# Optimization experiments

Hardware: AMD Instinct MI355X
Metric: run time of the kernel (lower is better)

Reference implementation:

```python
import jax, jax.numpy as jnp
import numpy as np

B, S, D, H, FF = 2, 2048, 1024, 16, 4096
DH = D // H
EPS = 1e-5


def rmsnorm(x, g):
    rms = jnp.sqrt(jnp.mean(x * x, axis=-1, keepdims=True) + EPS)
    return x / rms * g


def gelu(x):
    return x * 0.5 * (1.0 + jax.lax.erf(x / np.float32(np.sqrt(2.0))))


def setup_inputs() -> dict:
    key = jax.random.key(0)
    ks = jax.random.split(key, 9)
    sd = np.float32(1.0 / np.sqrt(D))
    sf = np.float32(1.0 / np.sqrt(FF))
    return {
        'x': jax.random.normal(ks[0], (B, S, D), jnp.float32),
        'wq': jax.random.normal(ks[1], (D, D), jnp.float32) * sd,
        'wk': jax.random.normal(ks[2], (D, D), jnp.float32) * sd,
        'wv': jax.random.normal(ks[3], (D, D), jnp.float32) * sd,
        'wo': jax.random.normal(ks[4], (D, D), jnp.float32) * sd,
        'w1': jax.random.normal(ks[5], (FF, D), jnp.float32) * sd,
        'w2': jax.random.normal(ks[6], (D, FF), jnp.float32) * sf,
        'g1': jax.random.uniform(ks[7], (D,), jnp.float32),
        'g2': jax.random.uniform(ks[8], (D,), jnp.float32),
    }


def reference(x, wq, wk, wv, wo, w1, w2, g1, g2):
    b, s, d = x.shape
    h = rmsnorm(x, g1)
    # torch Linear: y = x @ W.T ; split heads -> [b, s, H, DH]
    q = jnp.einsum('bsd,ed->bse', h, wq).reshape(b, s, H, DH)
    k = jnp.einsum('bsd,ed->bse', h, wk).reshape(b, s, H, DH)
    v = jnp.einsum('bsd,ed->bse', h, wv).reshape(b, s, H, DH)
    score = jnp.einsum('bqhd,bkhd->bhqk', q, k) / np.float32(np.sqrt(DH))
    causal = jnp.triu(jnp.ones((s, s), bool), 1)  # strictly upper = masked
    score = score + jnp.where(causal, jnp.float32(-1e9), jnp.float32(0.0))
    attn_w = jax.nn.softmax(score, axis=-1)
    o = jnp.einsum('bhqk,bkhd->bqhd', attn_w, v).reshape(b, s, d)
    attn_out = jnp.einsum('bsd,ed->bse', o, wo)
    x2 = attn_out + x
    h2 = rmsnorm(x2, g2)
    ffn = jnp.einsum('bsf,df->bsd', gelu(jnp.einsum('bsd,fd->bsf', h2, w1)), w2)
    return ffn + x2
```

## Files before the change

kernel.cpp:

```cpp
#include <hip/hip_runtime.h>
#include <cstdint>

#define B_ 2
#define S_ 2048
#define D_ 1024
#define H_ 16
#define DH_ 64
#define FF_ 4096
#define M_TOK (B_ * S_)

typedef __attribute__((ext_vector_type(8))) short short8;
typedef __attribute__((ext_vector_type(4))) float f32x4;
typedef __attribute__((ext_vector_type(4))) unsigned short us4;

typedef unsigned short u16;

#define SCL 0.18033688011112042f

__device__ __forceinline__ float bf2f(u16 u) {
  union { uint32_t u; float f; } x;
  x.u = ((uint32_t)u) << 16;
  return x.f;
}
__device__ __forceinline__ u16 f2bf(float f) {
  union { float f; uint32_t u; } x;
  x.f = f;
  uint32_t r = x.u + 0x7FFFu + ((x.u >> 16) & 1u);
  return (u16)(r >> 16);
}

__device__ __forceinline__ uint32_t pack2bf(float a, float b) {
  union { float f; uint32_t u; } x, y;
  x.f = a; y.f = b;
#if __has_builtin(__builtin_amdgcn_perm)
  return __builtin_amdgcn_perm(y.u + 0x8000u, x.u + 0x8000u, 0x07060302u);
#else
  return ((x.u + 0x8000u) >> 16) | ((y.u + 0x8000u) & 0xFFFF0000u);
#endif
}

__device__ __forceinline__ void gl_lds16(const void* g, void* l) {
  __builtin_amdgcn_global_load_lds(
      (const __attribute__((address_space(1))) uint32_t*)(uintptr_t)g,
      (__attribute__((address_space(3))) uint32_t*)(uintptr_t)l, 16, 0, 0);
}

__device__ __forceinline__ float gelu_f(float v) {
  const float y = 0.7978845608f * (v + 0.044715f * v * v * v);
  const float t = exp2f(y * 2.885390082f);
  const float th = 1.0f - 2.0f * __builtin_amdgcn_rcpf(t + 1.0f);
  return 0.5f * v * (1.0f + th);
}

#define MEG 1048576
#define PREP_CVT 12288

__global__ __launch_bounds__(256) void prep_k(const float* __restrict__ wq, const float* __restrict__ wk,
                                              const float* __restrict__ wv, const float* __restrict__ wo,
                                              const float* __restrict__ w1, const float* __restrict__ w2,
                                              u16* __restrict__ wqkv, u16* __restrict__ wob,
                                              u16* __restrict__ w1b, u16* __restrict__ w2b,
                                              const float* __restrict__ X, const float* __restrict__ G,
                                              u16* __restrict__ Hout) {
  __shared__ float red[4];
  const int bid = blockIdx.x;
  const int tid = threadIdx.x;
  if (bid < PREP_CVT) {
    const int n = (bid * 256 + tid) * 4;
    const float* src;
    u16* dst;
    int off;
    if (n < 3 * MEG) {
      dst = wqkv; off = n;
      src = (n < MEG) ? wq + n : (n < 2 * MEG ? wk + (n - MEG) : wv + (n - 2 * MEG));
    } else if (n < 4 * MEG) {
      dst = wob; off = n - 3 * MEG; src = wo + off;
    } else if (n < 8 * MEG) {
      dst = w1b; off = n - 4 * MEG; src = w1 + off;
    } else {
      dst = w2b; off = n - 8 * MEG; src = w2 + off;
    }
    const float4 v = *(const float4*)src;
    us4 o;
    o[0] = f2bf(v.x); o[1] = f2bf(v.y); o[2] = f2bf(v.z); o[3] = f2bf(v.w);
    *(us4*)&dst[off] = o;
  } else {
    const int row = bid - PREP_CVT;
    const float4 xx = *(const float4*)&X[(size_t)row * D_ + tid * 4];
    float v[4] = {xx.x, xx.y, xx.z, xx.w};
    float s = 0.f;
#pragma unroll
    for (int i = 0; i < 4; ++i) s += v[i] * v[i];
#pragma unroll
    for (int d = 1; d < 64; d <<= 1) s += __shfl_xor(s, d);
    if ((tid & 63) == 0) red[tid >> 6] = s;
    __syncthreads();
    s = red[0] + red[1] + red[2] + red[3];
    const float scale = rsqrtf(s * (1.0f / (float)D_) + 1e-5f);
    const float4 gg = *(const float4*)&G[tid * 4];
    us4 o;
    o[0] = f2bf(v[0] * scale * gg.x);
    o[1] = f2bf(v[1] * scale * gg.y);
    o[2] = f2bf(v[2] * scale * gg.z);
    o[3] = f2bf(v[3] * scale * gg.w);
    *(us4*)&Hout[(size_t)row * D_ + tid * 4] = o;
  }
}

__global__ __launch_bounds__(256) void rmsnorm_wo_k(const u16* __restrict__ P0, const u16* __restrict__ P1,
                                                    const float* __restrict__ X, const float* __restrict__ G,
                                                    float* __restrict__ X2, u16* __restrict__ Hout) {
  const int row = blockIdx.x;
  const int tid = threadIdx.x;
  const size_t off = (size_t)row * D_ + tid * 4;
  const us4 p0 = *(const us4*)&P0[off];
  const us4 p1 = *(const us4*)&P1[off];
  const float4 xx = *(const float4*)&X[off];
  float v[4];
  v[0] = bf2f(p0[0]) + bf2f(p1[0]) + xx.x;
  v[1] = bf2f(p0[1]) + bf2f(p1[1]) + xx.y;
  v[2] = bf2f(p0[2]) + bf2f(p1[2]) + xx.z;
  v[3] = bf2f(p0[3]) + bf2f(p1[3]) + xx.w;
  *(float4*)&X2[off] = float4{v[0], v[1], v[2], v[3]};
  float s = 0.f;
#pragma unroll
  for (int i = 0; i < 4; ++i) s += v[i] * v[i];
#pragma unroll
  for (int d = 1; d < 64; d <<= 1) s += __shfl_xor(s, d);
  __shared__ float red[4];
  if ((tid & 63) == 0) red[tid >> 6] = s;
  __syncthreads();
  s = red[0] + red[1] + red[2] + red[3];
  const float scale = rsqrtf(s * (1.0f / (float)D_) + 1e-5f);
  const float4 gg = *(const float4*)&G[tid * 4];
  us4 o;
  o[0] = f2bf(v[0] * scale * gg.x);
  o[1] = f2bf(v[1] * scale * gg.y);
  o[2] = f2bf(v[2] * scale * gg.z);
  o[3] = f2bf(v[3] * scale * gg.w);
  *(us4*)&Hout[off] = o;
}

__global__ __launch_bounds__(256) void ffn2_red_k(const u16* __restrict__ Q0, const u16* __restrict__ Q1,
                                                  float* __restrict__ OUT) {
  const int i = (blockIdx.x * 256 + threadIdx.x) * 4;
  const us4 a = *(const us4*)&Q0[i];
  const us4 b = *(const us4*)&Q1[i];
  const float4 c = *(const float4*)&OUT[i];
  *(float4*)&OUT[i] = float4{bf2f(a[0]) + bf2f(b[0]) + c.x, bf2f(a[1]) + bf2f(b[1]) + c.y,
                             bf2f(a[2]) + bf2f(b[2]) + c.z, bf2f(a[3]) + bf2f(b[3]) + c.w};
}

template <int MODE>
__global__ __launch_bounds__(256) void gemm_bt_k(const u16* __restrict__ A,
                                                 const u16* __restrict__ W,
                                                 u16* __restrict__ C0, u16* __restrict__ C1,
                                                 u16* __restrict__ C2, int N, int K) {
  __shared__ alignas(16) u16 As[256 * 32];
  __shared__ alignas(16) u16 Bs[256 * 32];
  const int tid = threadIdx.x;
  const int wv = tid >> 6, lane = tid & 63;
  const int r = lane & 15, quad = lane >> 4;
  const int nx = gridDim.x;
  const int nwg = nx * gridDim.y;
  const int orig = blockIdx.x + nx * blockIdx.y;
  const int id = (orig & 7) * (nwg >> 3) + (orig >> 3);
  const int bn = (id % nx) * 128;
  const int bm = (id / nx) * 128;
  const int row0 = (wv >> 1) * 64, col0 = (wv & 1) * 64;

  f32x4 acc[4][4] = {};

  int sm[4], sh[4], sg[4];
#pragma unroll
  for (int jj = 0; jj < 4; ++jj) {
    const int c = wv * 256 + jj * 64 + lane;
    const int lr = c >> 2;
    sm[jj] = lr & 127;
    sh[jj] = lr >> 7;
    sg[jj] = (c & 3) ^ ((sm[jj] >> 1) & 3);
  }

  for (int k0 = 0; k0 < K; k0 += 64) {
#pragma unroll
    for (int jj = 0; jj < 4; ++jj) {
      const int l0 = (wv * 256 + jj * 64) * 8;
      gl_lds16(&A[(size_t)(bm + sm[jj]) * K + k0 + sh[jj] * 32 + sg[jj] * 8], &As[l0]);
      gl_lds16(&W[(size_t)(bn + sm[jj]) * K + k0 + sh[jj] * 32 + sg[jj] * 8], &Bs[l0]);
    }
    __syncthreads();
#pragma unroll
    for (int h = 0; h < 2; ++h) {
      short8 af[4], bf[4];
#pragma unroll
      for (int mt = 0; mt < 4; ++mt) {
        const int mr = row0 + mt * 16 + r;
        af[mt] = *(const short8*)&As[(mr + 128 * h) * 32 + (quad ^ ((mr >> 1) & 3)) * 8];
      }
#pragma unroll
      for (int nt = 0; nt < 4; ++nt) {
        const int nr = col0 + nt * 16 + r;
        bf[nt] = *(const short8*)&Bs[(nr + 128 * h) * 32 + (quad ^ ((nr >> 1) & 3)) * 8];
      }
#pragma unroll
      for (int mt = 0; mt < 4; ++mt)
#pragma unroll
        for (int nt = 0; nt < 4; ++nt)
          acc[mt][nt] = __builtin_amdgcn_mfma_f32_16x16x32_bf16(af[mt], bf[nt], acc[mt][nt], 0, 0, 0);
    }
    __syncthreads();
  }

  if constexpr (MODE == 2) {
#pragma unroll
    for (int mt = 0; mt < 4; ++mt)
#pragma unroll
      for (int nt = 0; nt < 4; ++nt)
#pragma unroll
        for (int i = 0; i < 4; ++i) {
          const int grow = bm + row0 + mt * 16 + quad * 4 + i;
          const int gcol = bn + col0 + nt * 16 + r;
          C0[(size_t)grow * N + gcol] = f2bf(gelu_f(acc[mt][nt][i]));
        }
  } else {
    if (bn < 2048) {
#pragma unroll
      for (int mt = 0; mt < 4; ++mt) {
        const int grow0 = bm + row0 + mt * 16 + quad * 4;
#pragma unroll
        for (int nt = 0; nt < 4; ++nt) {
          const int gcol = bn + col0 + nt * 16 + r;
          u16* dst = (gcol < 1024) ? C0 : C1;
          const float sc = (gcol < 1024) ? SCL : 1.0f;
          const int cc = gcol & 1023;
#pragma unroll
          for (int i = 0; i < 4; ++i)
            dst[(size_t)(grow0 + i) * 1024 + cc] = f2bf(acc[mt][nt][i] * sc);
        }
      }
    } else {
#pragma unroll
      for (int mtp = 0; mtp < 4; mtp += 2) {
        const int tok0 = bm + row0 + mtp * 16 + quad * 4;
#pragma unroll
        for (int nt = 0; nt < 4; ++nt) {
          const int vcol = bn + col0 + nt * 16 + r - 2048;
          const size_t vtrow = (size_t)((tok0 >> 11) * 16 + (vcol >> 6)) * 64 + (vcol & 63);
#pragma unroll
          for (int i = 0; i < 4; ++i) {
            const int s = (tok0 + i) & 2047;
            const uint32_t pk =
                (uint32_t)f2bf(acc[mtp][nt][i]) | ((uint32_t)f2bf(acc[mtp + 1][nt][i]) << 16);
            *(uint32_t*)&C2[vtrow * 2048 + s + (s & 15)] = pk;
          }
        }
      }
    }
  }
}

__global__ __launch_bounds__(256) void gemm_sk2_k(const u16* __restrict__ A,
                                                  const u16* __restrict__ W,
                                                  u16* __restrict__ P0, u16* __restrict__ P1,
                                                  int N, int K, int KS) {
  __shared__ alignas(16) u16 As[256 * 32];
  __shared__ alignas(16) u16 Bs[256 * 32];
  const int tid = threadIdx.x;
  const int wv = tid >> 6, lane = tid & 63;
  const int r = lane & 15, quad = lane >> 4;
  const int orig = blockIdx.x + 8 * (blockIdx.y + 32 * blockIdx.z);
  const int id = (orig & 7) * 64 + (orig >> 3);
  const int bn = (id & 7) * 128;
  const int bm = ((id >> 3) & 31) * 128;
  const int bz = id >> 8;
  const int row0 = (wv >> 1) * 64, col0 = (wv & 1) * 64;
  const int koff = bz * KS;
  u16* P = bz ? P1 : P0;

  f32x4 acc[4][4] = {};

  int sm[4], sh[4], sg[4];
#pragma unroll
  for (int jj = 0; jj < 4; ++jj) {
    const int c = wv * 256 + jj * 64 + lane;
    const int lr = c >> 2;
    sm[jj] = lr & 127;
    sh[jj] = lr >> 7;
    sg[jj] = (c & 3) ^ ((sm[jj] >> 1) & 3);
  }

  for (int k0 = koff; k0 < koff + KS; k0 += 64) {
#pragma unroll
    for (int jj = 0; jj < 4; ++jj) {
      const int l0 = (wv * 256 + jj * 64) * 8;
      gl_lds16(&A[(size_t)(bm + sm[jj]) * K + k0 + sh[jj] * 32 + sg[jj] * 8], &As[l0]);
      gl_lds16(&W[(size_t)(bn + sm[jj]) * K + k0 + sh[jj] * 32 + sg[jj] * 8], &Bs[l0]);
    }
    __syncthreads();
#pragma unroll
    for (int h = 0; h < 2; ++h) {
      short8 af[4], bf[4];
#pragma unroll
      for (int mt = 0; mt < 4; ++mt) {
        const int mr = row0 + mt * 16 + r;
        af[mt] = *(const short8*)&As[(mr + 128 * h) * 32 + (quad ^ ((mr >> 1) & 3)) * 8];
      }
#pragma unroll
      for (int nt = 0; nt < 4; ++nt) {
        const int nr = col0 + nt * 16 + r;
        bf[nt] = *(const short8*)&Bs[(nr + 128 * h) * 32 + (quad ^ ((nr >> 1) & 3)) * 8];
      }
#pragma unroll
      for (int mt = 0; mt < 4; ++mt)
#pragma unroll
        for (int nt = 0; nt < 4; ++nt)
          acc[mt][nt] = __builtin_amdgcn_mfma_f32_16x16x32_bf16(af[mt], bf[nt], acc[mt][nt], 0, 0, 0);
    }
    __syncthreads();
  }

#pragma unroll
  for (int mt = 0; mt < 4; ++mt)
#pragma unroll
    for (int nt = 0; nt < 4; ++nt)
#pragma unroll
      for (int i = 0; i < 4; ++i) {
        const int grow = bm + row0 + mt * 16 + quad * 4 + i;
        const int gcol = bn + col0 + nt * 16 + r;
        P[(size_t)grow * N + gcol] = f2bf(acc[mt][nt][i]);
      }
}

#define ATTN_BODY(BUF, J0, RINK, RINV, ROUTK, ROUTV, DO_PF, DO_WR)                                 \
  {                                                                                                \
    __syncthreads();                                                                               \
    if (DO_PF) {                                                                                   \
      ROUTK = *(const short8*)&Kb[(size_t)((J0) + 64 + krow) * D_ + kg * 8];                       \
      ROUTV = *(const short8*)&VTb[(size_t)vrow * 2048 + (J0) + 64 + vg * 8];                      \
    }                                                                                              \
    f32x4 z[2][2];                                                                                 \
    __builtin_amdgcn_s_setprio(1);                                                                 \
    _Pragma("unroll") for (int kt = 0; kt < 2; ++kt) {                                             \
      const short8 kf0 = *(const short8*)&Ks[BUF][(kt * 16 + r) * 72 + quad * 8];                  \
      const short8 kf1 = *(const short8*)&Ks[BUF][(kt * 16 + r) * 72 + 32 + quad * 8];             \
      _Pragma("unroll") for (int f = 0; f < 2; ++f) {                                              \
        f32x4 zz = {};                                                                             \
        zz = __builtin_amdgcn_mfma_f32_16x16x32_bf16(qf[f][0], kf0, zz, 0, 0, 0);                  \
        zz = __builtin_amdgcn_mfma_f32_16x16x32_bf16(qf[f][1], kf1, zz, 0, 0, 0);                  \
        z[f][kt] = zz;                                                                             \
      }                                                                                            \
    }                                                                                              \
    __builtin_amdgcn_s_setprio(0);                                                                 \
    const bool masked = ((J0) + 31 > m0);                                                          \
    _Pragma("unroll") for (int f = 0; f < 2; ++f) _Pragma("unroll") for (int i = 0; i < 4; ++i) {  \
      const int qrow = m0 + f * 16 + quad * 4 + i;                                                 \
      float v0 = z[f][0][i];                                                                       \
      float v1 = z[f][1][i];                                                                       \
      if (masked) {                                                                                \
        if ((J0) + r > qrow) v0 = -128.f;                                                          \
        if ((J0) + 16 + r > qrow) v1 = -128.f;                                                     \
      }                                                                                            \
      *(uint32_t*)&Psw[(f * 16 + quad * 4 + i) * 40 + r * 2] = pack2bf(exp2f(v0), exp2f(v1));      \
    }                                                                                              \
    asm volatile("s_waitcnt lgkmcnt(0)" ::: "memory");                                             \
    short8 vf[4];                                                                                  \
    _Pragma("unroll") for (int nt = 0; nt < 4; ++nt)                                               \
        vf[nt] = *(const short8*)&Vs[BUF][(nt * 16 + r) * 40 + quad * 8];                          \
    __builtin_amdgcn_s_setprio(1);                                                                 \
    _Pragma("unroll") for (int f = 0; f < 2; ++f) {                                                \
      const short8 pf = *(const short8*)&Psw[(f * 16 + r) * 40 + quad * 8];                        \
      _Pragma("unroll") for (int nt = 0; nt < 4; ++nt)                                             \
          oacc[f][nt] = __builtin_amdgcn_mfma_f32_16x16x32_bf16(pf, vf[nt], oacc[f][nt], 0, 0, 0); \
      lacc[f] = __builtin_amdgcn_mfma_f32_16x16x32_bf16(pf, onesv, lacc[f], 0, 0, 0);              \
    }                                                                                              \
    __builtin_amdgcn_s_setprio(0);                                                                 \
    if (DO_WR) {                                                                                   \
      *(short8*)&Ks[(BUF) ^ 1][krow * 72 + kg * 8] = RINK;                                         \
      *(short8*)&Vs[(BUF) ^ 1][vrow * 40 + vg * 8] = RINV;                                         \
    }                                                                                              \
  }

__global__ __launch_bounds__(256, 2) void attn_k(const u16* __restrict__ Q,
                                                 const u16* __restrict__ Kx,
                                                 const u16* __restrict__ VT,
                                                 u16* __restrict__ O) {
  __shared__ alignas(16) u16 Ks[2][32 * 72];
  __shared__ alignas(16) u16 Vs[2][64 * 40];
  __shared__ alignas(16) u16 Ps[4][32 * 40];

  const int tid = threadIdx.x;
  const int wv = tid >> 6, lane = tid & 63;
  const int r = lane & 15, quad = lane >> 4;

  const int i_ = blockIdx.x + 16 * blockIdx.y;
  const int w = i_ >> 8;
  const int j = i_ & 255;
  const int xcd = j & 7;
  const int u = j >> 3;
  const int bh = xcd * 4 + (u >> 3);
  const int s = u & 7;
  const int bx = w ? s : (15 - s);
  const int b = bh >> 4, hh = bh & 15;

  const int niter = (bx + 1) * 4;
  const int m0 = bx * 128 + wv * 32;
  const size_t base = (size_t)b * S_ * D_ + (size_t)hh * DH_;
  const u16* Qb = Q + base;
  const u16* Kb = Kx + base;
  const u16* VTb = VT + (size_t)bh * 64 * 2048;
  u16* Psw = &Ps[wv][0];

  short8 qf[2][2];
#pragma unroll
  for (int f = 0; f < 2; ++f) {
    qf[f][0] = *(const short8*)&Qb[(size_t)(m0 + f * 16 + r) * D_ + quad * 8];
    qf[f][1] = *(const short8*)&Qb[(size_t)(m0 + f * 16 + r) * D_ + 32 + quad * 8];
  }

  short8 onesv;
#pragma unroll
  for (int e = 0; e < 8; ++e) onesv[e] = (short)0x3F80;

  f32x4 oacc[2][4] = {};
  f32x4 lacc[2] = {};

  const int krow = tid >> 3, kg = tid & 7;
  const int vrow = tid >> 2, vg = tid & 3;

  *(short8*)&Ks[0][krow * 72 + kg * 8] = *(const short8*)&Kb[(size_t)krow * D_ + kg * 8];
  *(short8*)&Vs[0][vrow * 40 + vg * 8] = *(const short8*)&VTb[(size_t)vrow * 2048 + vg * 8];
  short8 kA, vA, kB, vB;
  kA = *(const short8*)&Kb[(size_t)(32 + krow) * D_ + kg * 8];
  vA = *(const short8*)&VTb[(size_t)vrow * 2048 + 32 + vg * 8];

  for (int it = 0; it < niter; it += 2) {
    const int j0 = it * 32;
    ATTN_BODY(0, j0, kA, vA, kB, vB, (it + 2 < niter), true);
    ATTN_BODY(1, j0 + 32, kB, vB, kA, vA, (it + 3 < niter), (it + 2 < niter));
  }

#pragma unroll
  for (int f = 0; f < 2; ++f) {
#pragma unroll
    for (int i = 0; i < 4; ++i) {
      const int qrow = m0 + f * 16 + quad * 4 + i;
      const float linv = 1.0f / lacc[f][i];
#pragma unroll
      for (int nt = 0; nt < 4; ++nt)
        O[base + (size_t)qrow * D_ + nt * 16 + r] = f2bf(oacc[f][nt][i] * linv);
    }
  }
}

extern "C" void kernel_launch(void* const* d_in, const int* in_sizes, int n_in,
                              void* d_out, int out_size, void* d_ws, size_t ws_size,
                              hipStream_t stream) {
  (void)in_sizes; (void)n_in; (void)out_size; (void)ws_size;
  const float* x   = (const float*)d_in[0];
  const float* wq  = (const float*)d_in[1];
  const float* wk  = (const float*)d_in[2];
  const float* wvp = (const float*)d_in[3];
  const float* wo  = (const float*)d_in[4];
  const float* w1  = (const float*)d_in[5];
  const float* w2  = (const float*)d_in[6];
  const float* g1  = (const float*)d_in[7];
  const float* g2  = (const float*)d_in[8];
  float* out = (float*)d_out;

  u16* ws = (u16*)d_ws;
  const size_t TD = (size_t)M_TOK * D_;
  u16* h    = ws;
  u16* q    = ws + 1 * TD;
  u16* k    = ws + 2 * TD;
  u16* vt   = ws + 3 * TD;
  u16* h2   = ws + 4 * TD;
  u16* o    = h;
  u16* t    = ws;
  u16* P0   = q;
  u16* P1   = k;
  u16* Q0   = h2;
  u16* wqkv = ws + 5 * TD;
  u16* wob  = wqkv + 3 * MEG;
  u16* w1b  = wob + 1 * MEG;
  u16* w2b  = w1b + 4 * MEG;
  u16* Q1   = w2b + 4 * MEG;

  const dim3 blk(256);

  prep_k<<<PREP_CVT + M_TOK, blk, 0, stream>>>(wq, wk, wvp, wo, w1, w2, wqkv, wob, w1b, w2b,
                                               x, g1, h);
  gemm_bt_k<4><<<dim3(24, 32), blk, 0, stream>>>(h, wqkv, q, k, vt, 3072, 1024);
  attn_k<<<dim3(16, 32), blk, 0, stream>>>(q, k, vt, o);
  gemm_sk2_k<<<dim3(8, 32, 2), blk, 0, stream>>>(o, wob, P0, P1, 1024, 1024, 512);
  rmsnorm_wo_k<<<M_TOK, blk, 0, stream>>>(P0, P1, x, g2, out, h2);
  gemm_bt_k<2><<<dim3(32, 32), blk, 0, stream>>>(h2, w1b, t, nullptr, nullptr, 4096, 1024);
  gemm_sk2_k<<<dim3(8, 32, 2), blk, 0, stream>>>(t, w2b, Q0, Q1, 1024, 4096, 2048);
  ffn2_red_k<<<4096, blk, 0, stream>>>(Q0, Q1, out);
}
```

Before: 335.6 us.

## Double-buffer LDS tiles in GEMM kernels with async prefetch two steps ahead

Both GEMM kernels now use two LDS buffers per operand and issue the global-to-LDS loads for tile t+2 while computing on tile t. Completion is tracked with explicit vmcnt waits and raw barriers in place of full __syncthreads, and MFMA sections get raised wave priority through s_setprio. The aim is to hide global load latency behind matrix math. In exchange LDS use per block doubles to 64 KB, which may cut occupancy, and correctness now depends on the hand-set vmcnt counts matching the number of outstanding loads.

```diff
diff --git a/kernel.cpp b/kernel.cpp
--- a/kernel.cpp
+++ b/kernel.cpp
@@ -156,8 +156,8 @@
                                                  const u16* __restrict__ W,
                                                  u16* __restrict__ C0, u16* __restrict__ C1,
                                                  u16* __restrict__ C2, int N, int K) {
-  __shared__ alignas(16) u16 As[256 * 32];
-  __shared__ alignas(16) u16 Bs[256 * 32];
+  __shared__ alignas(16) u16 As[2][256 * 32];
+  __shared__ alignas(16) u16 Bs[2][256 * 32];
   const int tid = threadIdx.x;
   const int wv = tid >> 6, lane = tid & 63;
   const int r = lane & 15, quad = lane >> 4;
@@ -181,26 +181,40 @@
     sg[jj] = (c & 3) ^ ((sm[jj] >> 1) & 3);
   }
 
-  for (int k0 = 0; k0 < K; k0 += 64) {
+  const int NT = K >> 6;
+#pragma unroll
+  for (int jj = 0; jj < 4; ++jj) {
+    const int l0 = (wv * 256 + jj * 64) * 8;
+    gl_lds16(&A[(size_t)(bm + sm[jj]) * K + sh[jj] * 32 + sg[jj] * 8], &As[0][l0]);
+    gl_lds16(&W[(size_t)(bn + sm[jj]) * K + sh[jj] * 32 + sg[jj] * 8], &Bs[0][l0]);
+  }
+  if (NT > 1) {
 #pragma unroll
     for (int jj = 0; jj < 4; ++jj) {
       const int l0 = (wv * 256 + jj * 64) * 8;
-      gl_lds16(&A[(size_t)(bm + sm[jj]) * K + k0 + sh[jj] * 32 + sg[jj] * 8], &As[l0]);
-      gl_lds16(&W[(size_t)(bn + sm[jj]) * K + k0 + sh[jj] * 32 + sg[jj] * 8], &Bs[l0]);
-    }
-    __syncthreads();
+      gl_lds16(&A[(size_t)(bm + sm[jj]) * K + 64 + sh[jj] * 32 + sg[jj] * 8], &As[1][l0]);
+      gl_lds16(&W[(size_t)(bn + sm[jj]) * K + 64 + sh[jj] * 32 + sg[jj] * 8], &Bs[1][l0]);
+    }
+  }
+
+  for (int t = 0; t < NT; ++t) {
+    const int buf = t & 1;
+    if (t + 1 < NT) asm volatile("s_waitcnt vmcnt(8)" ::: "memory");
+    else            asm volatile("s_waitcnt vmcnt(0)" ::: "memory");
+    __builtin_amdgcn_s_barrier();
+    __builtin_amdgcn_s_setprio(1);
 #pragma unroll
     for (int h = 0; h < 2; ++h) {
       short8 af[4], bf[4];
 #pragma unroll
       for (int mt = 0; mt < 4; ++mt) {
         const int mr = row0 + mt * 16 + r;
-        af[mt] = *(const short8*)&As[(mr + 128 * h) * 32 + (quad ^ ((mr >> 1) & 3)) * 8];
+        af[mt] = *(const short8*)&As[buf][(mr + 128 * h) * 32 + (quad ^ ((mr >> 1) & 3)) * 8];
       }
 #pragma unroll
       for (int nt = 0; nt < 4; ++nt) {
         const int nr = col0 + nt * 16 + r;
-        bf[nt] = *(const short8*)&Bs[(nr + 128 * h) * 32 + (quad ^ ((nr >> 1) & 3)) * 8];
+        bf[nt] = *(const short8*)&Bs[buf][(nr + 128 * h) * 32 + (quad ^ ((nr >> 1) & 3)) * 8];
       }
 #pragma unroll
       for (int mt = 0; mt < 4; ++mt)
@@ -208,7 +222,17 @@
         for (int nt = 0; nt < 4; ++nt)
           acc[mt][nt] = __builtin_amdgcn_mfma_f32_16x16x32_bf16(af[mt], bf[nt], acc[mt][nt], 0, 0, 0);
     }
-    __syncthreads();
+    __builtin_amdgcn_s_setprio(0);
+    __builtin_amdgcn_s_barrier();
+    if (t + 2 < NT) {
+      const int k2 = (t + 2) << 6;
+#pragma unroll
+      for (int jj = 0; jj < 4; ++jj) {
+        const int l0 = (wv * 256 + jj * 64) * 8;
+        gl_lds16(&A[(size_t)(bm + sm[jj]) * K + k2 + sh[jj] * 32 + sg[jj] * 8], &As[buf][l0]);
+        gl_lds16(&W[(size_t)(bn + sm[jj]) * K + k2 + sh[jj] * 32 + sg[jj] * 8], &Bs[buf][l0]);
+      }
+    }
   }
 
   if constexpr (MODE == 2) {
@@ -263,8 +287,8 @@
                                                   const u16* __restrict__ W,
                                                   u16* __restrict__ P0, u16* __restrict__ P1,
                                                   int N, int K, int KS) {
-  __shared__ alignas(16) u16 As[256 * 32];
-  __shared__ alignas(16) u16 Bs[256 * 32];
+  __shared__ alignas(16) u16 As[2][256 * 32];
+  __shared__ alignas(16) u16 Bs[2][256 * 32];
   const int tid = threadIdx.x;
   const int wv = tid >> 6, lane = tid & 63;
   const int r = lane & 15, quad = lane >> 4;
@@ -289,26 +313,40 @@
     sg[jj] = (c & 3) ^ ((sm[jj] >> 1) & 3);
   }
 
-  for (int k0 = koff; k0 < koff + KS; k0 += 64) {
+  const int NT = KS >> 6;
+#pragma unroll
+  for (int jj = 0; jj < 4; ++jj) {
+    const int l0 = (wv * 256 + jj * 64) * 8;
+    gl_lds16(&A[(size_t)(bm + sm[jj]) * K + koff + sh[jj] * 32 + sg[jj] * 8], &As[0][l0]);
+    gl_lds16(&W[(size_t)(bn + sm[jj]) * K + koff + sh[jj] * 32 + sg[jj] * 8], &Bs[0][l0]);
+  }
+  if (NT > 1) {
 #pragma unroll
     for (int jj = 0; jj < 4; ++jj) {
       const int l0 = (wv * 256 + jj * 64) * 8;
-      gl_lds16(&A[(size_t)(bm + sm[jj]) * K + k0 + sh[jj] * 32 + sg[jj] * 8], &As[l0]);
-      gl_lds16(&W[(size_t)(bn + sm[jj]) * K + k0 + sh[jj] * 32 + sg[jj] * 8], &Bs[l0]);
-    }
-    __syncthreads();
+      gl_lds16(&A[(size_t)(bm + sm[jj]) * K + koff + 64 + sh[jj] * 32 + sg[jj] * 8], &As[1][l0]);
+      gl_lds16(&W[(size_t)(bn + sm[jj]) * K + koff + 64 + sh[jj] * 32 + sg[jj] * 8], &Bs[1][l0]);
+    }
+  }
+
+  for (int t = 0; t < NT; ++t) {
+    const int buf = t & 1;
+    if (t + 1 < NT) asm volatile("s_waitcnt vmcnt(8)" ::: "memory");
+    else            asm volatile("s_waitcnt vmcnt(0)" ::: "memory");
+    __builtin_amdgcn_s_barrier();
+    __builtin_amdgcn_s_setprio(1);
 #pragma unroll
     for (int h = 0; h < 2; ++h) {
       short8 af[4], bf[4];
 #pragma unroll
       for (int mt = 0; mt < 4; ++mt) {
         const int mr = row0 + mt * 16 + r;
-        af[mt] = *(const short8*)&As[(mr + 128 * h) * 32 + (quad ^ ((mr >> 1) & 3)) * 8];
+        af[mt] = *(const short8*)&As[buf][(mr + 128 * h) * 32 + (quad ^ ((mr >> 1) & 3)) * 8];
       }
 #pragma unroll
       for (int nt = 0; nt < 4; ++nt) {
         const int nr = col0 + nt * 16 + r;
-        bf[nt] = *(const short8*)&Bs[(nr + 128 * h) * 32 + (quad ^ ((nr >> 1) & 3)) * 8];
+        bf[nt] = *(const short8*)&Bs[buf][(nr + 128 * h) * 32 + (quad ^ ((nr >> 1) & 3)) * 8];
       }
 #pragma unroll
       for (int mt = 0; mt < 4; ++mt)
@@ -316,7 +354,17 @@
         for (int nt = 0; nt < 4; ++nt)
           acc[mt][nt] = __builtin_amdgcn_mfma_f32_16x16x32_bf16(af[mt], bf[nt], acc[mt][nt], 0, 0, 0);
     }
-    __syncthreads();
+    __builtin_amdgcn_s_setprio(0);
+    __builtin_amdgcn_s_barrier();
+    if (t + 2 < NT) {
+      const int k2 = koff + ((t + 2) << 6);
+#pragma unroll
+      for (int jj = 0; jj < 4; ++jj) {
+        const int l0 = (wv * 256 + jj * 64) * 8;
+        gl_lds16(&A[(size_t)(bm + sm[jj]) * K + k2 + sh[jj] * 32 + sg[jj] * 8], &As[buf][l0]);
+        gl_lds16(&W[(size_t)(bn + sm[jj]) * K + k2 + sh[jj] * 32 + sg[jj] * 8], &Bs[buf][l0]);
+      }
+    }
   }
 
 #pragma unroll
```

After: 313.9 us (median of 2 runs). -6.5%, faster.
